# Optimization experiments

Measured on AMD Instinct MI355X. Metric: run time of the kernel, lower is better.

## Reference

```python
import jax, jax.numpy as jnp
import numpy as np

B, S, D, H, DFF = 4, 2048, 1024, 16, 4096
DK = D // H
EPS = 1e-6


def setup_inputs() -> dict:
    key = jax.random.key(0)
    ks = jax.random.split(key, 8)
    s = 0.02
    return {
        "x": jax.random.normal(ks[0], (B, S, D), jnp.float32),
        "src_mask": jnp.ones((B, 1, 1, S), jnp.int32),
        "w_q": jax.random.normal(ks[1], (D, D), jnp.float32) * s,
        "w_k": jax.random.normal(ks[2], (D, D), jnp.float32) * s,
        "w_v": jax.random.normal(ks[3], (D, D), jnp.float32) * s,
        "w_o": jax.random.normal(ks[4], (D, D), jnp.float32) * s,
        "w1": jax.random.normal(ks[5], (DFF, D), jnp.float32) * s,
        "b1": jnp.zeros((DFF,), jnp.float32),
        "w2": jax.random.normal(ks[6], (D, DFF), jnp.float32) * s,
        "b2": jnp.zeros((D,), jnp.float32),
        "gamma1": jnp.ones((1,), jnp.float32),
        "beta1": jnp.zeros((1,), jnp.float32),
        "gamma2": jnp.ones((1,), jnp.float32),
        "beta2": jnp.zeros((1,), jnp.float32),
    }


def layernorm(x, gamma, beta):
    # matches torch source: unbiased std (ddof=1), eps added to std, scalar gamma/beta
    mean = jnp.mean(x, axis=-1, keepdims=True)
    std = jnp.std(x, axis=-1, keepdims=True, ddof=1)
    return gamma * (x - mean) / (std + EPS) + beta


def mha(x, w_q, w_k, w_v, w_o):
    # Linear(bias=False): y = x @ W.T
    q = (x @ w_q.T).reshape(B, S, H, DK).transpose(0, 2, 1, 3)  # [B,H,S,DK]
    k = (x @ w_k.T).reshape(B, S, H, DK).transpose(0, 2, 1, 3)
    v = (x @ w_v.T).reshape(B, S, H, DK).transpose(0, 2, 1, 3)
    scores = jnp.einsum('bhqd,bhkd->bhqk', q, k) / np.float32(np.sqrt(DK))
    # NOTE: source calls attention.masked_fill(...) without assigning the result,
    # so the mask has no effect; faithfully replicated (mask unused).
    attn = jax.nn.softmax(scores, axis=-1)
    ctx = jnp.einsum('bhqk,bhkd->bhqd', attn, v)  # [B,H,S,DK]
    ctx = ctx.transpose(0, 2, 1, 3).reshape(B, S, D)
    return ctx @ w_o.T


def ffn(x, w1, b1, w2, b2):
    return jax.nn.relu(x @ w1.T + b1) @ w2.T + b2


def reference(x, src_mask, w_q, w_k, w_v, w_o, w1, b1, w2, b2,
              gamma1, beta1, gamma2, beta2):
    # pre-norm residual blocks; dropout is identity in eval
    x = x + mha(layernorm(x, gamma1, beta1), w_q, w_k, w_v, w_o)
    x = x + ffn(layernorm(x, gamma2, beta2), w1, b1, w2, b2)
    return x
```

## Files before the change

### kernel.cpp

```cpp
#include <hip/hip_runtime.h>
#include <hip/hip_bf16.h>

#define DEV static __device__ __forceinline__

typedef unsigned short u16;
typedef float fp32x4 __attribute__((ext_vector_type(4)));
typedef short bf16x8 __attribute__((ext_vector_type(8)));
typedef short bf16x4 __attribute__((ext_vector_type(4)));

DEV float bf2f(u16 u) { return __uint_as_float(((unsigned)u) << 16); }
DEV u16 f2bf(float f) {
  unsigned x = __float_as_uint(f);
  x += 0x7fffu + ((x >> 16) & 1u);
  return (u16)(x >> 16);
}

DEV void gload_lds16(const void* g, void* l) {
  __builtin_amdgcn_global_load_lds(
      (__attribute__((address_space(1))) void*)(unsigned long long)g,
      (__attribute__((address_space(3))) void*)(unsigned int)(unsigned long long)l,
      16, 0, 0);
}

__global__ __launch_bounds__(256) void cvt_kernel(const float* __restrict__ in,
                                                  u16* __restrict__ out) {
  const int i = blockIdx.x * 256 + threadIdx.x;
  const fp32x4 v = ((const fp32x4*)in)[i];
  bf16x4 o;
#pragma unroll
  for (int j = 0; j < 4; j++) o[j] = (short)f2bf(v[j]);
  ((bf16x4*)out)[i] = o;
}

__global__ __launch_bounds__(256) void ln_kernel(const float* __restrict__ x,
                                                 u16* __restrict__ y,
                                                 const float* __restrict__ gamma,
                                                 const float* __restrict__ beta) {
  const int row = blockIdx.x;
  const int t = threadIdx.x;
  const fp32x4 v = ((const fp32x4*)(x + (size_t)row * 1024))[t];
  float s = v[0] + v[1] + v[2] + v[3];
  float ss = v[0] * v[0] + v[1] * v[1] + v[2] * v[2] + v[3] * v[3];
#pragma unroll
  for (int o = 32; o > 0; o >>= 1) {
    s += __shfl_down(s, o);
    ss += __shfl_down(ss, o);
  }
  __shared__ float rs[4], rss[4];
  const int w = t >> 6;
  if ((t & 63) == 0) { rs[w] = s; rss[w] = ss; }
  __syncthreads();
  const float S = rs[0] + rs[1] + rs[2] + rs[3];
  const float SS = rss[0] + rss[1] + rss[2] + rss[3];
  const float mean = S * (1.0f / 1024.0f);
  const float var = fmaxf((SS - 1024.0f * mean * mean) * (1.0f / 1023.0f), 0.0f);
  const float sc = gamma[0] / (sqrtf(var) + 1e-6f);
  const float be = beta[0];
  bf16x4 o;
#pragma unroll
  for (int j = 0; j < 4; j++) o[j] = (short)f2bf((v[j] - mean) * sc + be);
  ((bf16x4*)(y + (size_t)row * 1024))[t] = o;
}

template <int EPI>
__global__ __launch_bounds__(256, 2) void gemm_bt(
    const u16* __restrict__ A, const u16* __restrict__ W, u16* __restrict__ Cb,
    float* __restrict__ Cf, const float* __restrict__ bias,
    const float* __restrict__ resid, int M, int N, int K) {
  __shared__ u16 sA[128 * 32];
  __shared__ u16 sB[128 * 32];
  const int t = threadIdx.x;
  const int lane = t & 63;
  const int w = t >> 6;
  const int wr = (w >> 1) * 64;
  const int wc = (w & 1) * 64;
  const int lr = lane & 15;
  const int hi = lane >> 4;
  const int bx = blockIdx.x, by = blockIdx.y;

  const u16* gA = A + (size_t)(by * 128 + (t >> 2)) * K + (t & 3) * 8;
  const u16* gB = W + (size_t)(bx * 128 + (t >> 2)) * K + (t & 3) * 8;
  const size_t rstep = (size_t)64 * K;
  u16* lA = &sA[t * 8];
  u16* lB = &sB[t * 8];

  const fp32x4 zero4 = {0.f, 0.f, 0.f, 0.f};
  fp32x4 acc[4][4];
#pragma unroll
  for (int i = 0; i < 4; i++)
#pragma unroll
    for (int j = 0; j < 4; j++) acc[i][j] = zero4;

  for (int k0 = 0; k0 < K; k0 += 32) {
    gload_lds16(gA, lA);
    gload_lds16(gA + rstep, lA + 2048);
    gload_lds16(gB, lB);
    gload_lds16(gB + rstep, lB + 2048);
    gA += 32;
    gB += 32;
    __syncthreads();
    bf16x8 af[4], bfr[4];
#pragma unroll
    for (int i = 0; i < 4; i++)
      af[i] = *(const bf16x8*)&sA[(wr + i * 16 + lr) * 32 + hi * 8];
#pragma unroll
    for (int j = 0; j < 4; j++)
      bfr[j] = *(const bf16x8*)&sB[(wc + j * 16 + lr) * 32 + hi * 8];
#pragma unroll
    for (int i = 0; i < 4; i++)
#pragma unroll
      for (int j = 0; j < 4; j++)
        acc[i][j] =
            __builtin_amdgcn_mfma_f32_16x16x32_bf16(af[i], bfr[j], acc[i][j], 0, 0, 0);
    __syncthreads();
  }

  const int row0 = by * 128 + wr + hi * 4;
  const int col0 = bx * 128 + wc + lr;
  float bj[4] = {0.f, 0.f, 0.f, 0.f};
  if (EPI == 1 || EPI == 3) {
#pragma unroll
    for (int j = 0; j < 4; j++) bj[j] = bias[col0 + j * 16];
  }
#pragma unroll
  for (int i = 0; i < 4; i++) {
#pragma unroll
    for (int r = 0; r < 4; r++) {
      const size_t row = (size_t)(row0 + i * 16 + r);
#pragma unroll
      for (int j = 0; j < 4; j++) {
        const int col = col0 + j * 16;
        float v = acc[i][j][r];
        if (EPI == 1) v = fmaxf(v + bj[j], 0.f);
        if (EPI == 3) v += bj[j];
        if (EPI >= 2) {
          v += resid[row * N + col];
          Cf[row * N + col] = v;
        } else {
          Cb[row * N + col] = f2bf(v);
        }
      }
    }
  }
}

__global__ __launch_bounds__(256) void vtrans_kernel(const u16* __restrict__ V,
                                                     u16* __restrict__ VT) {
  const int st = blockIdx.x;
  const int h = blockIdx.y;
  const int b = blockIdx.z;
  const int t = threadIdx.x;
  const int r = t >> 2, c0 = (t & 3) * 16;
  __shared__ u16 sT[64][72];

  const u16* src = V + ((size_t)(b * 2048 + st * 64 + r)) * 1024 + h * 64 + c0;
  bf16x8 v0 = *(const bf16x8*)src;
  bf16x8 v1 = *(const bf16x8*)(src + 8);
  const int cb = c0 ^ ((r >> 4) << 4);
  *(bf16x8*)&sT[r][cb] = v0;
  *(bf16x8*)&sT[r][cb + 8] = v1;
  __syncthreads();

  const int dc = r ^ ((c0 >> 4) << 4);
  bf16x8 o0, o1;
#pragma unroll
  for (int i = 0; i < 8; i++) o0[i] = sT[c0 + i][dc];
#pragma unroll
  for (int i = 0; i < 8; i++) o1[i] = sT[c0 + 8 + i][dc];
  u16* dst = VT + ((size_t)((b * 16 + h) * 64 + r)) * 2048 + st * 64 + c0;
  *(bf16x8*)dst = o0;
  *(bf16x8*)(dst + 8) = o1;
}

__global__ __launch_bounds__(256, 2) void attn_kernel(const u16* __restrict__ Q,
                                                      const u16* __restrict__ K,
                                                      const u16* __restrict__ VT,
                                                      u16* __restrict__ O) {
  const int qt = blockIdx.x;
  const int h = blockIdx.y;
  const int b = blockIdx.z;
  const int t = threadIdx.x, lane = t & 63, w = t >> 6;
  const int lr = lane & 15, hi = lane >> 4;

  __shared__ u16 sK[64][72];
  __shared__ u16 sVT[64][72];
  __shared__ u16 sQP[64][72];

  const size_t base = ((size_t)b * 2048) * 1024 + (size_t)h * 64;
  const size_t vbase = (((size_t)b * 16 + h) * 64) * 2048;
  const int r = t >> 2, c0 = (t & 3) * 16;

  {
    const u16* src = Q + base + (size_t)(qt * 64 + r) * 1024 + c0;
    bf16x8 u0 = *(const bf16x8*)src;
    bf16x8 u1 = *(const bf16x8*)(src + 8);
#pragma unroll
    for (int i = 0; i < 8; i++) sQP[r][c0 + i] = f2bf(bf2f((u16)u0[i]) * 0.125f);
#pragma unroll
    for (int i = 0; i < 8; i++) sQP[r][c0 + 8 + i] = f2bf(bf2f((u16)u1[i]) * 0.125f);
  }
  __syncthreads();
  bf16x8 qreg0 = *(const bf16x8*)&sQP[w * 16 + lr][hi * 8];
  bf16x8 qreg1 = *(const bf16x8*)&sQP[w * 16 + lr][32 + hi * 8];

  bf16x8 kA, kB, vA, vB;
  {
    const u16* ks = K + base + (size_t)r * 1024 + c0;
    kA = *(const bf16x8*)ks;
    kB = *(const bf16x8*)(ks + 8);
    const u16* vs = VT + vbase + (size_t)r * 2048 + c0;
    vA = *(const bf16x8*)vs;
    vB = *(const bf16x8*)(vs + 8);
  }

  const fp32x4 zero4 = {0.f, 0.f, 0.f, 0.f};
  fp32x4 onT[4];
#pragma unroll
  for (int df = 0; df < 4; df++) onT[df] = zero4;
  float mrun = -1e30f, lrun = 0.f;

  for (int kt = 0; kt < 32; ++kt) {
    __syncthreads();
    *(bf16x8*)&sK[r][c0] = kA;
    *(bf16x8*)&sK[r][c0 + 8] = kB;
    *(bf16x8*)&sVT[r][c0] = vA;
    *(bf16x8*)&sVT[r][c0 + 8] = vB;
    __syncthreads();
    if (kt < 31) {
      const u16* kn = K + base + (size_t)((kt + 1) * 64 + r) * 1024 + c0;
      kA = *(const bf16x8*)kn;
      kB = *(const bf16x8*)(kn + 8);
      const u16* vn = VT + vbase + (size_t)r * 2048 + (kt + 1) * 64 + c0;
      vA = *(const bf16x8*)vn;
      vB = *(const bf16x8*)(vn + 8);
    }

    fp32x4 sc[4];
#pragma unroll
    for (int kk = 0; kk < 4; kk++) {
      fp32x4 a = zero4;
      bf16x8 kf0 = *(const bf16x8*)&sK[kk * 16 + lr][hi * 8];
      bf16x8 kf1 = *(const bf16x8*)&sK[kk * 16 + lr][32 + hi * 8];
      a = __builtin_amdgcn_mfma_f32_16x16x32_bf16(kf0, qreg0, a, 0, 0, 0);
      a = __builtin_amdgcn_mfma_f32_16x16x32_bf16(kf1, qreg1, a, 0, 0, 0);
      sc[kk] = a;
    }

    float mloc = -1e30f;
#pragma unroll
    for (int kk = 0; kk < 4; kk++)
#pragma unroll
      for (int rr = 0; rr < 4; rr++) mloc = fmaxf(mloc, sc[kk][rr]);
    mloc = fmaxf(mloc, __shfl_xor(mloc, 16));
    mloc = fmaxf(mloc, __shfl_xor(mloc, 32));
    const float mnew = fmaxf(mrun, mloc);
    const float alpha = __expf(mrun - mnew);
    float psum = 0.f;
#pragma unroll
    for (int kk = 0; kk < 4; kk++) {
      bf16x4 pv;
#pragma unroll
      for (int rr = 0; rr < 4; rr++) {
        const float p = __expf(sc[kk][rr] - mnew);
        psum += p;
        pv[rr] = (short)f2bf(p);
      }
      *(bf16x4*)&sQP[w * 16 + lr][kk * 16 + hi * 4] = pv;
    }
    psum += __shfl_xor(psum, 16);
    psum += __shfl_xor(psum, 32);
    lrun = lrun * alpha + psum;
    mrun = mnew;
#pragma unroll
    for (int df = 0; df < 4; df++) onT[df] *= alpha;

#pragma unroll
    for (int df = 0; df < 4; df++) {
#pragma unroll
      for (int ks = 0; ks < 2; ks++) {
        bf16x8 vf = *(const bf16x8*)&sVT[df * 16 + lr][ks * 32 + hi * 8];
        bf16x8 pf = *(const bf16x8*)&sQP[w * 16 + lr][ks * 32 + hi * 8];
        onT[df] = __builtin_amdgcn_mfma_f32_16x16x32_bf16(vf, pf, onT[df], 0, 0, 0);
      }
    }
  }

  const float invl = 1.0f / lrun;
  u16* dst = O + base + (size_t)(qt * 64 + w * 16 + lr) * 1024;
#pragma unroll
  for (int df = 0; df < 4; df++) {
    bf16x4 o4;
#pragma unroll
    for (int rr = 0; rr < 4; rr++) o4[rr] = (short)f2bf(onT[df][rr] * invl);
    *(bf16x4*)&dst[df * 16 + hi * 4] = o4;
  }
}

extern "C" void kernel_launch(void* const* d_in, const int* in_sizes, int n_in,
                              void* d_out, int out_size, void* d_ws, size_t ws_size,
                              hipStream_t stream) {
  const float* x = (const float*)d_in[0];
  const float* wq = (const float*)d_in[2];
  const float* wk = (const float*)d_in[3];
  const float* wv = (const float*)d_in[4];
  const float* wo = (const float*)d_in[5];
  const float* w1 = (const float*)d_in[6];
  const float* b1 = (const float*)d_in[7];
  const float* w2 = (const float*)d_in[8];
  const float* b2 = (const float*)d_in[9];
  const float* g1 = (const float*)d_in[10];
  const float* be1 = (const float*)d_in[11];
  const float* g2 = (const float*)d_in[12];
  const float* be2 = (const float*)d_in[13];
  float* out = (float*)d_out;

  const size_t MB = 1024ull * 1024ull;
  char* ws = (char*)d_ws;
  if (ws_size < 136 * MB) return;

  u16* wqb = (u16*)(ws + 0 * MB);
  u16* wkb = (u16*)(ws + 2 * MB);
  u16* wvb = (u16*)(ws + 4 * MB);
  u16* wob = (u16*)(ws + 6 * MB);
  u16* w1b = (u16*)(ws + 8 * MB);
  u16* w2b = (u16*)(ws + 16 * MB);
  u16* Qb = (u16*)(ws + 24 * MB);
  u16* Kb = (u16*)(ws + 40 * MB);
  u16* Vb = (u16*)(ws + 56 * MB);
  u16* Ctx = (u16*)(ws + 72 * MB);
  u16* Hb = (u16*)(ws + 24 * MB);
  u16* Yb = (u16*)(ws + 88 * MB);
  u16* VTb = (u16*)(ws + 88 * MB);
  float* X2 = (float*)(ws + 104 * MB);

  dim3 blk(256);

  cvt_kernel<<<1024, blk, 0, stream>>>(wq, wqb);
  cvt_kernel<<<1024, blk, 0, stream>>>(wk, wkb);
  cvt_kernel<<<1024, blk, 0, stream>>>(wv, wvb);
  cvt_kernel<<<1024, blk, 0, stream>>>(wo, wob);
  cvt_kernel<<<4096, blk, 0, stream>>>(w1, w1b);
  cvt_kernel<<<4096, blk, 0, stream>>>(w2, w2b);

  ln_kernel<<<8192, blk, 0, stream>>>(x, Yb, g1, be1);

  gemm_bt<0><<<dim3(8, 64), blk, 0, stream>>>(Yb, wqb, Qb, nullptr, nullptr, nullptr,
                                              8192, 1024, 1024);
  gemm_bt<0><<<dim3(8, 64), blk, 0, stream>>>(Yb, wkb, Kb, nullptr, nullptr, nullptr,
                                              8192, 1024, 1024);
  gemm_bt<0><<<dim3(8, 64), blk, 0, stream>>>(Yb, wvb, Vb, nullptr, nullptr, nullptr,
                                              8192, 1024, 1024);
  vtrans_kernel<<<dim3(32, 16, 4), blk, 0, stream>>>(Vb, VTb);

  attn_kernel<<<dim3(32, 16, 4), blk, 0, stream>>>(Qb, Kb, VTb, Ctx);

  gemm_bt<2><<<dim3(8, 64), blk, 0, stream>>>(Ctx, wob, nullptr, X2, nullptr, x, 8192,
                                              1024, 1024);

  ln_kernel<<<8192, blk, 0, stream>>>(X2, Yb, g2, be2);

  gemm_bt<1><<<dim3(32, 64), blk, 0, stream>>>(Yb, w1b, Hb, nullptr, b1, nullptr, 8192,
                                               4096, 1024);

  gemm_bt<3><<<dim3(8, 64), blk, 0, stream>>>(Hb, w2b, nullptr, out, b2, X2, 8192, 1024,
                                              4096);
}
```

Before: 499.7 us.

## Remap workgroups across XCDs, use exp2 softmax, packed bf16 converts and setprio

Workgroup IDs in the GEMM and the attention kernel are remapped so that consecutive logical tiles land on the same XCD, aiming for better L2 reuse of shared operands. The attention softmax folds log2(e) into the Q scale and uses exp2f instead of __expf. The manual bf16 rounding is replaced by the hardware v_cvt_pk_bf16_f32 instruction for Q, P and the output. s_setprio is raised around the MFMA blocks. The remap assumes the grid size is a multiple of 8, and the packed conversion may round slightly differently from the manual round-to-nearest-even.

```diff
diff --git a/kernel.cpp b/kernel.cpp
--- a/kernel.cpp
+++ b/kernel.cpp
@@ -13,6 +13,12 @@
   unsigned x = __float_as_uint(f);
   x += 0x7fffu + ((x >> 16) & 1u);
   return (u16)(x >> 16);
+}
+
+DEV unsigned cvt_pk_bf16(float a, float b) {
+  unsigned r;
+  asm("v_cvt_pk_bf16_f32 %0, %1, %2" : "=v"(r) : "v"(a), "v"(b));
+  return r;
 }
 
 DEV void gload_lds16(const void* g, void* l) {
@@ -76,7 +82,12 @@
   const int wc = (w & 1) * 64;
   const int lr = lane & 15;
   const int hi = lane >> 4;
-  const int bx = blockIdx.x, by = blockIdx.y;
+
+  const int nwgx = gridDim.x;
+  const int orig = blockIdx.y * nwgx + blockIdx.x;
+  const int cpx = (nwgx * gridDim.y) >> 3;
+  const int logical = (orig & 7) * cpx + (orig >> 3);
+  const int bx = logical % nwgx, by = logical / nwgx;
 
   const u16* gA = A + (size_t)(by * 128 + (t >> 2)) * K + (t & 3) * 8;
   const u16* gB = W + (size_t)(bx * 128 + (t >> 2)) * K + (t & 3) * 8;
@@ -176,9 +187,12 @@
                                                       const u16* __restrict__ K,
                                                       const u16* __restrict__ VT,
                                                       u16* __restrict__ O) {
-  const int qt = blockIdx.x;
-  const int h = blockIdx.y;
-  const int b = blockIdx.z;
+  const int orig = blockIdx.x + 32 * (blockIdx.y + 16 * blockIdx.z);
+  const int logical = (orig & 7) * 256 + (orig >> 3);
+  const int qt = logical & 31;
+  const int h = (logical >> 5) & 15;
+  const int b = logical >> 9;
+
   const int t = threadIdx.x, lane = t & 63, w = t >> 6;
   const int lr = lane & 15, hi = lane >> 4;
 
@@ -191,17 +205,24 @@
   const int r = t >> 2, c0 = (t & 3) * 16;
 
   {
+    const float qs = 0.125f * 1.44269504f;
     const u16* src = Q + base + (size_t)(qt * 64 + r) * 1024 + c0;
     bf16x8 u0 = *(const bf16x8*)src;
     bf16x8 u1 = *(const bf16x8*)(src + 8);
-#pragma unroll
-    for (int i = 0; i < 8; i++) sQP[r][c0 + i] = f2bf(bf2f((u16)u0[i]) * 0.125f);
-#pragma unroll
-    for (int i = 0; i < 8; i++) sQP[r][c0 + 8 + i] = f2bf(bf2f((u16)u1[i]) * 0.125f);
+    union { unsigned u[4]; bf16x8 v; } q0, q1;
+#pragma unroll
+    for (int j = 0; j < 4; j++)
+      q0.u[j] = cvt_pk_bf16(bf2f((u16)u0[2 * j]) * qs, bf2f((u16)u0[2 * j + 1]) * qs);
+#pragma unroll
+    for (int j = 0; j < 4; j++)
+      q1.u[j] = cvt_pk_bf16(bf2f((u16)u1[2 * j]) * qs, bf2f((u16)u1[2 * j + 1]) * qs);
+    *(bf16x8*)&sQP[r][c0] = q0.v;
+    *(bf16x8*)&sQP[r][c0 + 8] = q1.v;
   }
   __syncthreads();
-  bf16x8 qreg0 = *(const bf16x8*)&sQP[w * 16 + lr][hi * 8];
-  bf16x8 qreg1 = *(const bf16x8*)&sQP[w * 16 + lr][32 + hi * 8];
+  const int qrow = w * 16 + lr;
+  bf16x8 qreg0 = *(const bf16x8*)&sQP[qrow][hi * 8];
+  bf16x8 qreg1 = *(const bf16x8*)&sQP[qrow][32 + hi * 8];
 
   bf16x8 kA, kB, vA, vB;
   {
@@ -236,6 +257,7 @@
     }
 
     fp32x4 sc[4];
+    __builtin_amdgcn_s_setprio(1);
 #pragma unroll
     for (int kk = 0; kk < 4; kk++) {
       fp32x4 a = zero4;
@@ -245,6 +267,7 @@
       a = __builtin_amdgcn_mfma_f32_16x16x32_bf16(kf1, qreg1, a, 0, 0, 0);
       sc[kk] = a;
     }
+    __builtin_amdgcn_s_setprio(0);
 
     float mloc = -1e30f;
 #pragma unroll
@@ -254,18 +277,15 @@
     mloc = fmaxf(mloc, __shfl_xor(mloc, 16));
     mloc = fmaxf(mloc, __shfl_xor(mloc, 32));
     const float mnew = fmaxf(mrun, mloc);
-    const float alpha = __expf(mrun - mnew);
+    const float alpha = exp2f(mrun - mnew);
     float psum = 0.f;
 #pragma unroll
     for (int kk = 0; kk < 4; kk++) {
-      bf16x4 pv;
-#pragma unroll
-      for (int rr = 0; rr < 4; rr++) {
-        const float p = __expf(sc[kk][rr] - mnew);
-        psum += p;
-        pv[rr] = (short)f2bf(p);
-      }
-      *(bf16x4*)&sQP[w * 16 + lr][kk * 16 + hi * 4] = pv;
+      float p0 = exp2f(sc[kk][0] - mnew), p1 = exp2f(sc[kk][1] - mnew);
+      float p2 = exp2f(sc[kk][2] - mnew), p3 = exp2f(sc[kk][3] - mnew);
+      psum += (p0 + p1) + (p2 + p3);
+      uint2 pk = {cvt_pk_bf16(p0, p1), cvt_pk_bf16(p2, p3)};
+      *(uint2*)&sQP[qrow][kk * 16 + hi * 4] = pk;
     }
     psum += __shfl_xor(psum, 16);
     psum += __shfl_xor(psum, 32);
@@ -274,25 +294,26 @@
 #pragma unroll
     for (int df = 0; df < 4; df++) onT[df] *= alpha;
 
+    __builtin_amdgcn_s_setprio(1);
 #pragma unroll
     for (int df = 0; df < 4; df++) {
 #pragma unroll
       for (int ks = 0; ks < 2; ks++) {
         bf16x8 vf = *(const bf16x8*)&sVT[df * 16 + lr][ks * 32 + hi * 8];
-        bf16x8 pf = *(const bf16x8*)&sQP[w * 16 + lr][ks * 32 + hi * 8];
+        bf16x8 pf = *(const bf16x8*)&sQP[qrow][ks * 32 + hi * 8];
         onT[df] = __builtin_amdgcn_mfma_f32_16x16x32_bf16(vf, pf, onT[df], 0, 0, 0);
       }
     }
+    __builtin_amdgcn_s_setprio(0);
   }
 
   const float invl = 1.0f / lrun;
-  u16* dst = O + base + (size_t)(qt * 64 + w * 16 + lr) * 1024;
+  u16* dst = O + base + (size_t)(qt * 64 + qrow) * 1024;
 #pragma unroll
   for (int df = 0; df < 4; df++) {
-    bf16x4 o4;
-#pragma unroll
-    for (int rr = 0; rr < 4; rr++) o4[rr] = (short)f2bf(onT[df][rr] * invl);
-    *(bf16x4*)&dst[df * 16 + hi * 4] = o4;
+    uint2 o2 = {cvt_pk_bf16(onT[df][0] * invl, onT[df][1] * invl),
+                cvt_pk_bf16(onT[df][2] * invl, onT[df][3] * invl)};
+    *(uint2*)&dst[df * 16 + hi * 4] = o2;
   }
 }
 
```

New measurement: 475.5 us. -4.8%, faster.
